# Kernel tuning notes

Measured on AMD Instinct MI355X. Metric: run time of the kernel, lower is better.

The kernel has to match this reference:

```python
import jax, jax.numpy as jnp
import numpy as np

HID = 768
HEADS = 12
HEAD_LEN = HID // HEADS
SCALE_INV = 1.0 / np.sqrt(HEAD_LEN).astype(np.float32)


def setup_inputs() -> dict:
    key = jax.random.key(0)
    ks = jax.random.split(key, 5)
    std = 1.0 / np.sqrt(HID)
    return {
        "x": jax.random.normal(ks[0], (1, 4096, HID), dtype=jnp.float32),
        "w_q": jax.random.normal(ks[1], (HID, HID), dtype=jnp.float32) * std,
        "w_k": jax.random.normal(ks[2], (HID, HID), dtype=jnp.float32) * std,
        "w_v": jax.random.normal(ks[3], (HID, HID), dtype=jnp.float32) * std,
        "w_fc": jax.random.normal(ks[4], (HID, HID), dtype=jnp.float32) * std,
    }


def reference(x, w_q, w_k, w_v, w_fc):
    B, S, D = x.shape
    # torch Linear weight layout [out, in]: y = x @ W.T
    def proj_heads(w):
        y = jnp.einsum("bsd,ed->bse", x, w)
        return y.reshape(B, S, HEADS, HEAD_LEN).transpose(0, 2, 1, 3)  # bhsd
    q = proj_heads(w_q)
    k = proj_heads(w_k)
    v = proj_heads(w_v)
    scores = SCALE_INV * jnp.einsum("bhqd,bhkd->bhqk", q, k)
    attn = jax.nn.softmax(scores, axis=-1)
    out = jnp.einsum("bhqk,bhkd->bhqd", attn, v)
    out = out.transpose(0, 2, 1, 3).reshape(B, S, D)
    return jnp.einsum("bsd,ed->bse", out, w_fc)
```

## Files before the change

kernel.cpp:

```cpp
#include <hip/hip_runtime.h>
#include <hip/hip_bf16.h>

#define S_LEN 4096
#define HID 768
#define NHEAD 12
#define HL 64

typedef __attribute__((ext_vector_type(8))) short short8;
typedef __attribute__((ext_vector_type(4))) float f32x4;
using bf16 = __hip_bfloat16;

__device__ __forceinline__ void gl2lds16(const void* g, void* l) {
  __builtin_amdgcn_global_load_lds((__attribute__((address_space(1))) void*)(g),
                                   (__attribute__((address_space(3))) void*)(l),
                                   16, 0, 0);
}

__device__ __forceinline__ f32x4 mfma_bf16(short8 a, short8 b, f32x4 c) {
  return __builtin_amdgcn_mfma_f32_16x16x32_bf16(a, b, c, 0, 0, 0);
}

__device__ __forceinline__ void storeC(float* C, long idx, float v) { C[idx] = v; }
__device__ __forceinline__ void storeC(bf16* C, long idx, float v) { C[idx] = __float2bfloat16(v); }

#define BAR() asm volatile("s_waitcnt lgkmcnt(0)\n\ts_barrier" ::: "memory")
#define BAR_VM(n) \
  asm volatile("s_waitcnt vmcnt(" #n ") lgkmcnt(0)\n\ts_barrier" ::: "memory")

__global__ __launch_bounds__(256) void cvt_all(
    const float* __restrict__ x, const float* __restrict__ wq,
    const float* __restrict__ wk, const float* __restrict__ wv,
    const float* __restrict__ wfc, bf16* __restrict__ xb, bf16* __restrict__ wqb,
    bf16* __restrict__ wkb, bf16* __restrict__ wvb, bf16* __restrict__ wfcb) {
  const long NX = (long)S_LEN * HID;
  const long NW = (long)HID * HID;
  long i = ((long)blockIdx.x * 256 + threadIdx.x) * 4;
  const float* src;
  bf16* dst;
  long off;
  if (i < NX) {
    src = x; dst = xb; off = i;
  } else {
    long j = i - NX;
    int wsel = (int)(j / NW);
    off = j - (long)wsel * NW;
    src = wsel == 0 ? wq : wsel == 1 ? wk : wsel == 2 ? wv : wfc;
    dst = wsel == 0 ? wqb : wsel == 1 ? wkb : wsel == 2 ? wvb : wfcb;
  }
  float4 v = *(const float4*)(src + off);
  bf16 h0 = __float2bfloat16(v.x), h1 = __float2bfloat16(v.y);
  bf16 h2 = __float2bfloat16(v.z), h3 = __float2bfloat16(v.w);
  ushort4 o;
  o.x = *(unsigned short*)&h0; o.y = *(unsigned short*)&h1;
  o.z = *(unsigned short*)&h2; o.w = *(unsigned short*)&h3;
  *(ushort4*)(dst + off) = o;
}

template <typename OT>
__global__ __launch_bounds__(256, 3) void gemm_bt(
    const bf16* __restrict__ A, const bf16* __restrict__ B0,
    const bf16* __restrict__ B1, const bf16* __restrict__ B2,
    OT* __restrict__ C0, OT* __restrict__ C1, OT* __restrict__ C2, float qscale) {
  constexpr int K = HID, NK = K / 32;
  __shared__ __align__(16) bf16 As[3][128 * 32];
  __shared__ __align__(16) bf16 Bs[3][128 * 32];
  const int z = blockIdx.z;
  const bf16* B = (z == 0) ? B0 : (z == 1) ? B1 : B2;
  OT* C = (z == 0) ? C0 : (z == 1) ? C1 : C2;
  const float sc = (z == 0) ? qscale : 1.0f;
  const int bm = blockIdx.y, bn = blockIdx.x;
  const int t = threadIdx.x, lane = t & 63, w = t >> 6;
  const int wm = w >> 1, wn = w & 1;
  const int q4 = lane >> 4, c16 = lane & 15;
  const int srow = lane >> 2, scol = (lane & 3) * 8;
  const bf16* Ab = A + (long)bm * 128 * K;
  const bf16* Bb = B + (long)bn * 128 * K;

  auto stage = [&](int k, int buf) {
#pragma unroll
    for (int r = 0; r < 2; ++r) {
      int rowb = r * 64 + w * 16;
      gl2lds16(Ab + (long)(rowb + srow) * K + k * 32 + scol, &As[buf][rowb * 32]);
      gl2lds16(Bb + (long)(rowb + srow) * K + k * 32 + scol, &Bs[buf][rowb * 32]);
    }
  };

  f32x4 acc[4][4] = {};
  stage(0, 0);
  stage(1, 1);
  for (int k = 0; k < NK; ++k) {
    if (k < NK - 1) BAR_VM(4); else BAR_VM(0);
    if (k + 2 < NK) stage(k + 2, (k + 2) % 3);
    const bf16* Al = As[k % 3];
    const bf16* Bl = Bs[k % 3];
    short8 af[4], bfv[4];
#pragma unroll
    for (int i = 0; i < 4; ++i)
      af[i] = *(const short8*)&Al[(wm * 64 + i * 16 + c16) * 32 + q4 * 8];
#pragma unroll
    for (int j = 0; j < 4; ++j)
      bfv[j] = *(const short8*)&Bl[(wn * 64 + j * 16 + c16) * 32 + q4 * 8];
#pragma unroll
    for (int i = 0; i < 4; ++i)
#pragma unroll
      for (int j = 0; j < 4; ++j)
        acc[i][j] = mfma_bf16(af[i], bfv[j], acc[i][j]);
  }
  const long crow0 = (long)bm * 128 + wm * 64;
  const int ccol0 = bn * 128 + wn * 64;
#pragma unroll
  for (int i = 0; i < 4; ++i)
#pragma unroll
    for (int j = 0; j < 4; ++j)
#pragma unroll
      for (int r = 0; r < 4; ++r) {
        long row = crow0 + i * 16 + q4 * 4 + r;
        int col = ccol0 + j * 16 + c16;
        storeC(C, row * HID + col, sc * acc[i][j][r]);
      }
}

__global__ __launch_bounds__(256, 3) void gemm_fc(const bf16* __restrict__ A,
                                                  const bf16* __restrict__ B,
                                                  float* __restrict__ C) {
  constexpr int NK = HID / 32;
  __shared__ __align__(16) bf16 As[3][64 * 32];
  __shared__ __align__(16) bf16 Bs[3][64 * 32];
  const int bm = blockIdx.y, bn = blockIdx.x;
  const int t = threadIdx.x, lane = t & 63, w = t >> 6;
  const int wm = w >> 1, wn = w & 1;
  const int q4 = lane >> 4, c16 = lane & 15;
  const int srow = lane >> 2, scol = (lane & 3) * 8;
  const bf16* Ab = A + (long)bm * 64 * HID;
  const bf16* Bb = B + (long)bn * 64 * HID;

  auto stage = [&](int k, int buf) {
    gl2lds16(Ab + (long)(w * 16 + srow) * HID + k * 32 + scol,
             &As[buf][w * 16 * 32]);
    gl2lds16(Bb + (long)(w * 16 + srow) * HID + k * 32 + scol,
             &Bs[buf][w * 16 * 32]);
  };

  f32x4 acc[2][2] = {};
  stage(0, 0);
  stage(1, 1);
  for (int k = 0; k < NK; ++k) {
    if (k < NK - 1) BAR_VM(2); else BAR_VM(0);
    if (k + 2 < NK) stage(k + 2, (k + 2) % 3);
    const bf16* Al = As[k % 3];
    const bf16* Bl = Bs[k % 3];
    short8 af[2], bfv[2];
#pragma unroll
    for (int i = 0; i < 2; ++i)
      af[i] = *(const short8*)&Al[(wm * 32 + i * 16 + c16) * 32 + q4 * 8];
#pragma unroll
    for (int j = 0; j < 2; ++j)
      bfv[j] = *(const short8*)&Bl[(wn * 32 + j * 16 + c16) * 32 + q4 * 8];
#pragma unroll
    for (int i = 0; i < 2; ++i)
#pragma unroll
      for (int j = 0; j < 2; ++j)
        acc[i][j] = mfma_bf16(af[i], bfv[j], acc[i][j]);
  }
#pragma unroll
  for (int i = 0; i < 2; ++i)
#pragma unroll
    for (int j = 0; j < 2; ++j)
#pragma unroll
      for (int r = 0; r < 4; ++r) {
        long row = (long)bm * 64 + wm * 32 + i * 16 + q4 * 4 + r;
        int col = bn * 64 + wn * 32 + j * 16 + c16;
        C[row * HID + col] = acc[i][j][r];
      }
}

__global__ __launch_bounds__(256) void transpose_v(const bf16* __restrict__ V,
                                                   bf16* __restrict__ Vt) {
  __shared__ unsigned short tile[64][65];
  const int bs = blockIdx.x * 64;
  const int be = blockIdx.y * 64;
  const int t = threadIdx.x;
#pragma unroll
  for (int p = 0; p < 4; ++p) {
    int i = p * 256 + t;
    int r = i >> 4;
    int c = (i & 15) * 4;
    ushort4 v = *(const ushort4*)((const unsigned short*)V + (long)(bs + r) * HID + be + c);
    tile[r][c] = v.x; tile[r][c + 1] = v.y; tile[r][c + 2] = v.z; tile[r][c + 3] = v.w;
  }
  __syncthreads();
#pragma unroll
  for (int p = 0; p < 4; ++p) {
    int i = p * 256 + t;
    int r = i >> 4;
    int c = (i & 15) * 4;
    ushort4 v;
    v.x = tile[c][r]; v.y = tile[c + 1][r]; v.z = tile[c + 2][r]; v.w = tile[c + 3][r];
    *(ushort4*)((unsigned short*)Vt + (long)(be + r) * S_LEN + bs + c) = v;
  }
}

__global__ __launch_bounds__(256, 3) void flash_attn(const bf16* __restrict__ Q,
                                                     const bf16* __restrict__ Kg,
                                                     const bf16* __restrict__ Vt,
                                                     bf16* __restrict__ O) {
  __shared__ __align__(16) bf16 Ps[2][64 * 128];
  __shared__ float Lred[4][64];
  const int qt = blockIdx.x, h = blockIdx.y;
  const int t = threadIdx.x, lane = t & 63, w = t >> 6;
  const int q4 = lane >> 4, c16 = lane & 15;
  const int s0 = qt * 64;

  short8 qf[2][4];
  {
    const bf16* Qb = Q + (long)(s0 + c16) * HID + h * HL + q4 * 8;
#pragma unroll
    for (int j = 0; j < 4; ++j)
#pragma unroll
      for (int ks = 0; ks < 2; ++ks)
        qf[ks][j] = *(const short8*)(Qb + (long)j * 16 * HID + ks * 32);
  }
  const bf16* kp = Kg + (long)(w * 32 + c16) * HID + h * HL + q4 * 8;
  const bf16* vp = Vt + (long)(h * HL + w * 16 + c16) * S_LEN + q4 * 8;

  float l_part[4] = {0.f, 0.f, 0.f, 0.f};
  f32x4 o_acc[4] = {};
  short8 kf[2][2], vf[4];
#pragma unroll
  for (int rr = 0; rr < 2; ++rr)
#pragma unroll
    for (int ks = 0; ks < 2; ++ks)
      kf[rr][ks] = *(const short8*)(kp + (long)rr * 16 * HID + ks * 32);
#pragma unroll
  for (int kc = 0; kc < 4; ++kc) vf[kc] = *(const short8*)(vp + kc * 32);

  for (int kt = 0; kt < S_LEN / 128; ++kt) {
    bf16* Pb = Ps[kt & 1];
    f32x4 sacc[2][4] = {};
#pragma unroll
    for (int rr = 0; rr < 2; ++rr)
#pragma unroll
      for (int ks = 0; ks < 2; ++ks)
#pragma unroll
        for (int j = 0; j < 4; ++j)
          sacc[rr][j] = mfma_bf16(kf[rr][ks], qf[ks][j], sacc[rr][j]);

    const bf16* kpn = (kt == S_LEN / 128 - 1) ? kp : kp + 128 * HID;
#pragma unroll
    for (int rr = 0; rr < 2; ++rr)
#pragma unroll
      for (int ks = 0; ks < 2; ++ks)
        kf[rr][ks] = *(const short8*)(kpn + (long)rr * 16 * HID + ks * 32);
    kp = kpn;

#pragma unroll
    for (int rr = 0; rr < 2; ++rr) {
      const int wch = ((w * 4 + rr * 2 + (q4 >> 1)));
#pragma unroll
      for (int j = 0; j < 4; ++j) {
        float p0 = __builtin_amdgcn_exp2f(sacc[rr][j][0]);
        float p1 = __builtin_amdgcn_exp2f(sacc[rr][j][1]);
        float p2 = __builtin_amdgcn_exp2f(sacc[rr][j][2]);
        float p3 = __builtin_amdgcn_exp2f(sacc[rr][j][3]);
        l_part[j] += (p0 + p1) + (p2 + p3);
        __hip_bfloat162 a01 = __float22bfloat162_rn(float2{p0, p1});
        __hip_bfloat162 a23 = __float22bfloat162_rn(float2{p2, p3});
        int2 pk;
        pk.x = *(int*)&a01;
        pk.y = *(int*)&a23;
        *(int2*)&Pb[(j * 16 + c16) * 128 + (wch ^ c16) * 8 + (q4 & 1) * 4] = pk;
      }
    }
    BAR();

#pragma unroll
    for (int kc = 0; kc < 4; ++kc) {
#pragma unroll
      for (int j = 0; j < 4; ++j) {
        short8 pf = *(const short8*)&Pb[(j * 16 + c16) * 128 + ((kc * 4 + q4) ^ c16) * 8];
        o_acc[j] = mfma_bf16(vf[kc], pf, o_acc[j]);
      }
    }
    const bf16* vpn = (kt == S_LEN / 128 - 1) ? vp : vp + 128;
#pragma unroll
    for (int kc = 0; kc < 4; ++kc) vf[kc] = *(const short8*)(vpn + kc * 32);
    vp = vpn;
  }

#pragma unroll
  for (int j = 0; j < 4; ++j) {
    float s = l_part[j];
    s += __shfl_xor(s, 16, 64);
    s += __shfl_xor(s, 32, 64);
    Lred[w][j * 16 + c16] = s;
  }
  __syncthreads();
#pragma unroll
  for (int j = 0; j < 4; ++j) {
    int q = j * 16 + c16;
    float lt = Lred[0][q] + Lred[1][q] + Lred[2][q] + Lred[3][q];
    float rl = 1.0f / lt;
    float v0 = o_acc[j][0] * rl, v1 = o_acc[j][1] * rl;
    float v2 = o_acc[j][2] * rl, v3 = o_acc[j][3] * rl;
    bf16 b0 = __float2bfloat16(v0), b1 = __float2bfloat16(v1);
    bf16 b2 = __float2bfloat16(v2), b3 = __float2bfloat16(v3);
    short4 pk;
    pk.x = *(short*)&b0; pk.y = *(short*)&b1; pk.z = *(short*)&b2; pk.w = *(short*)&b3;
    *(short4*)&O[(long)(s0 + q) * HID + h * HL + w * 16 + q4 * 4] = pk;
  }
}

extern "C" void kernel_launch(void* const* d_in, const int* in_sizes, int n_in,
                              void* d_out, int out_size, void* d_ws, size_t ws_size,
                              hipStream_t stream) {
  const float* x = (const float*)d_in[0];
  const float* wq = (const float*)d_in[1];
  const float* wk = (const float*)d_in[2];
  const float* wv = (const float*)d_in[3];
  const float* wfc = (const float*)d_in[4];
  float* out = (float*)d_out;

  const long NBIG = (long)S_LEN * HID * sizeof(bf16);
  const long NWB = (long)HID * HID * sizeof(bf16);
  char* p = (char*)d_ws;
  bf16* xb = (bf16*)p;   p += NBIG;
  bf16* wqb = (bf16*)p;  p += NWB;
  bf16* wkb = (bf16*)p;  p += NWB;
  bf16* wvb = (bf16*)p;  p += NWB;
  bf16* wfcb = (bf16*)p; p += NWB;
  bf16* Qb = (bf16*)p;   p += NBIG;
  bf16* Kb = (bf16*)p;   p += NBIG;
  bf16* Vb = (bf16*)p;   p += NBIG;
  bf16* Vtb = (bf16*)p;  p += NBIG;
  bf16* Ob = (bf16*)p;   p += NBIG;

  const float c1 = 0.125f * 1.44269504088896340736f;

  const long total4 = ((long)S_LEN * HID + 4L * HID * HID) / 4;
  cvt_all<<<(int)(total4 / 256), 256, 0, stream>>>(x, wq, wk, wv, wfc, xb, wqb, wkb,
                                                   wvb, wfcb);
  gemm_bt<bf16><<<dim3(HID / 128, S_LEN / 128, 3), 256, 0, stream>>>(
      xb, wqb, wkb, wvb, Qb, Kb, Vb, c1);
  transpose_v<<<dim3(S_LEN / 64, HID / 64), 256, 0, stream>>>(Vb, Vtb);
  flash_attn<<<dim3(S_LEN / 64, NHEAD), 256, 0, stream>>>(Qb, Kb, Vtb, Ob);
  gemm_fc<<<dim3(HID / 64, S_LEN / 64), 256, 0, stream>>>(Ob, wfcb, out);
}
```

Baseline: 213.3 us.

## Make P tile wave-private to drop per-iteration block barrier in flash attention

Each wave now owns its own 32-key slice of the K tile and computes the PV product over all 64 head dims for those keys, keeping P in a wave-private LDS buffer. This removes the block-wide barrier and the shared double-buffered P tile from the inner loop. The cost is four times as many output accumulators per wave (more registers, with risk to occupancy at 3 blocks per CU) and a cross-wave LDS reduction of partial outputs at the end.

```diff
diff --git a/kernel.cpp b/kernel.cpp
--- a/kernel.cpp
+++ b/kernel.cpp
@@ -23,7 +23,6 @@
 __device__ __forceinline__ void storeC(float* C, long idx, float v) { C[idx] = v; }
 __device__ __forceinline__ void storeC(bf16* C, long idx, float v) { C[idx] = __float2bfloat16(v); }
 
-#define BAR() asm volatile("s_waitcnt lgkmcnt(0)\n\ts_barrier" ::: "memory")
 #define BAR_VM(n) \
   asm volatile("s_waitcnt vmcnt(" #n ") lgkmcnt(0)\n\ts_barrier" ::: "memory")
 
@@ -200,16 +199,18 @@
   }
 }
 
+#define PSTR 36
 __global__ __launch_bounds__(256, 3) void flash_attn(const bf16* __restrict__ Q,
                                                      const bf16* __restrict__ Kg,
                                                      const bf16* __restrict__ Vt,
                                                      bf16* __restrict__ O) {
-  __shared__ __align__(16) bf16 Ps[2][64 * 128];
+  __shared__ __align__(16) char PsRaw[4 * 64 * PSTR * sizeof(bf16)];
   __shared__ float Lred[4][64];
   const int qt = blockIdx.x, h = blockIdx.y;
   const int t = threadIdx.x, lane = t & 63, w = t >> 6;
   const int q4 = lane >> 4, c16 = lane & 15;
   const int s0 = qt * 64;
+  bf16* Pw = (bf16*)PsRaw + w * 64 * PSTR;
 
   short8 qf[2][4];
   {
@@ -221,10 +222,10 @@
         qf[ks][j] = *(const short8*)(Qb + (long)j * 16 * HID + ks * 32);
   }
   const bf16* kp = Kg + (long)(w * 32 + c16) * HID + h * HL + q4 * 8;
-  const bf16* vp = Vt + (long)(h * HL + w * 16 + c16) * S_LEN + q4 * 8;
+  const bf16* vp = Vt + (long)(h * HL + c16) * S_LEN + w * 32 + q4 * 8;
 
   float l_part[4] = {0.f, 0.f, 0.f, 0.f};
-  f32x4 o_acc[4] = {};
+  f32x4 acc[4][4] = {};
   short8 kf[2][2], vf[4];
 #pragma unroll
   for (int rr = 0; rr < 2; ++rr)
@@ -232,58 +233,53 @@
     for (int ks = 0; ks < 2; ++ks)
       kf[rr][ks] = *(const short8*)(kp + (long)rr * 16 * HID + ks * 32);
 #pragma unroll
-  for (int kc = 0; kc < 4; ++kc) vf[kc] = *(const short8*)(vp + kc * 32);
+  for (int dt = 0; dt < 4; ++dt)
+    vf[dt] = *(const short8*)(vp + (long)dt * 16 * S_LEN);
 
   for (int kt = 0; kt < S_LEN / 128; ++kt) {
-    bf16* Pb = Ps[kt & 1];
-    f32x4 sacc[2][4] = {};
-#pragma unroll
-    for (int rr = 0; rr < 2; ++rr)
+    const bf16* kpn = (kt == S_LEN / 128 - 1) ? kp : kp + 128 * HID;
+#pragma unroll
+    for (int rr = 0; rr < 2; ++rr) {
+      f32x4 sacc[4] = {};
 #pragma unroll
       for (int ks = 0; ks < 2; ++ks)
 #pragma unroll
         for (int j = 0; j < 4; ++j)
-          sacc[rr][j] = mfma_bf16(kf[rr][ks], qf[ks][j], sacc[rr][j]);
-
-    const bf16* kpn = (kt == S_LEN / 128 - 1) ? kp : kp + 128 * HID;
-#pragma unroll
-    for (int rr = 0; rr < 2; ++rr)
+          sacc[j] = mfma_bf16(kf[rr][ks], qf[ks][j], sacc[j]);
 #pragma unroll
       for (int ks = 0; ks < 2; ++ks)
         kf[rr][ks] = *(const short8*)(kpn + (long)rr * 16 * HID + ks * 32);
-    kp = kpn;
-
-#pragma unroll
-    for (int rr = 0; rr < 2; ++rr) {
-      const int wch = ((w * 4 + rr * 2 + (q4 >> 1)));
 #pragma unroll
       for (int j = 0; j < 4; ++j) {
-        float p0 = __builtin_amdgcn_exp2f(sacc[rr][j][0]);
-        float p1 = __builtin_amdgcn_exp2f(sacc[rr][j][1]);
-        float p2 = __builtin_amdgcn_exp2f(sacc[rr][j][2]);
-        float p3 = __builtin_amdgcn_exp2f(sacc[rr][j][3]);
+        float p0 = __builtin_amdgcn_exp2f(sacc[j][0]);
+        float p1 = __builtin_amdgcn_exp2f(sacc[j][1]);
+        float p2 = __builtin_amdgcn_exp2f(sacc[j][2]);
+        float p3 = __builtin_amdgcn_exp2f(sacc[j][3]);
         l_part[j] += (p0 + p1) + (p2 + p3);
         __hip_bfloat162 a01 = __float22bfloat162_rn(float2{p0, p1});
         __hip_bfloat162 a23 = __float22bfloat162_rn(float2{p2, p3});
         int2 pk;
         pk.x = *(int*)&a01;
         pk.y = *(int*)&a23;
-        *(int2*)&Pb[(j * 16 + c16) * 128 + (wch ^ c16) * 8 + (q4 & 1) * 4] = pk;
+        *(int2*)&Pw[(j * 16 + c16) * PSTR + rr * 16 + q4 * 4] = pk;
       }
     }
-    BAR();
-
-#pragma unroll
-    for (int kc = 0; kc < 4; ++kc) {
-#pragma unroll
-      for (int j = 0; j < 4; ++j) {
-        short8 pf = *(const short8*)&Pb[(j * 16 + c16) * 128 + ((kc * 4 + q4) ^ c16) * 8];
-        o_acc[j] = mfma_bf16(vf[kc], pf, o_acc[j]);
-      }
-    }
+    kp = kpn;
+
+    short8 pf[4];
+#pragma unroll
+    for (int j = 0; j < 4; ++j)
+      pf[j] = *(const short8*)&Pw[(j * 16 + c16) * PSTR + q4 * 8];
+#pragma unroll
+    for (int dt = 0; dt < 4; ++dt)
+#pragma unroll
+      for (int j = 0; j < 4; ++j)
+        acc[dt][j] = mfma_bf16(vf[dt], pf[j], acc[dt][j]);
+
     const bf16* vpn = (kt == S_LEN / 128 - 1) ? vp : vp + 128;
 #pragma unroll
-    for (int kc = 0; kc < 4; ++kc) vf[kc] = *(const short8*)(vpn + kc * 32);
+    for (int dt = 0; dt < 4; ++dt)
+      vf[dt] = *(const short8*)(vpn + (long)dt * 16 * S_LEN);
     vp = vpn;
   }
 
@@ -295,18 +291,29 @@
     Lred[w][j * 16 + c16] = s;
   }
   __syncthreads();
-#pragma unroll
-  for (int j = 0; j < 4; ++j) {
-    int q = j * 16 + c16;
-    float lt = Lred[0][q] + Lred[1][q] + Lred[2][q] + Lred[3][q];
-    float rl = 1.0f / lt;
-    float v0 = o_acc[j][0] * rl, v1 = o_acc[j][1] * rl;
-    float v2 = o_acc[j][2] * rl, v3 = o_acc[j][3] * rl;
-    bf16 b0 = __float2bfloat16(v0), b1 = __float2bfloat16(v1);
-    bf16 b2 = __float2bfloat16(v2), b3 = __float2bfloat16(v3);
+  const int qmy = w * 16 + c16;
+  const float rl =
+      1.0f / (Lred[0][qmy] + Lred[1][qmy] + Lred[2][qmy] + Lred[3][qmy]);
+  float* Osc = (float*)PsRaw;
+#pragma unroll
+  for (int dt = 0; dt < 4; ++dt) {
+    __syncthreads();
+#pragma unroll
+    for (int j = 0; j < 4; ++j)
+      *(f32x4*)&Osc[(w * 64 + j * 16 + c16) * 16 + q4 * 4] = acc[dt][j];
+    __syncthreads();
+    f32x4 s = *(const f32x4*)&Osc[(0 * 64 + qmy) * 16 + q4 * 4];
+#pragma unroll
+    for (int ww = 1; ww < 4; ++ww) {
+      f32x4 p = *(const f32x4*)&Osc[(ww * 64 + qmy) * 16 + q4 * 4];
+#pragma unroll
+      for (int r = 0; r < 4; ++r) s[r] += p[r];
+    }
+    bf16 b0 = __float2bfloat16(s[0] * rl), b1 = __float2bfloat16(s[1] * rl);
+    bf16 b2 = __float2bfloat16(s[2] * rl), b3 = __float2bfloat16(s[3] * rl);
     short4 pk;
     pk.x = *(short*)&b0; pk.y = *(short*)&b1; pk.z = *(short*)&b2; pk.w = *(short*)&b3;
-    *(short4*)&O[(long)(s0 + q) * HID + h * HL + w * 16 + q4 * 4] = pk;
+    *(short4*)&O[(long)(s0 + qmy) * HID + h * HL + dt * 16 + q4 * 4] = pk;
   }
 }
 
```

Measured after the change: 258.3 us. +21.1%, slower.
